# Performance work log

Hardware: AMD Instinct MI355X
Metric: run time of the kernel (lower is better)

## Reference

```python
import jax, jax.numpy as jnp
import numpy as np
import math

B, S, E = 2, 2048, 2048
H, NOPE, ROPE, V, KVR, DOWN = 16, 64, 32, 64, 256, 2
QKD = NOPE + ROPE
SCALE = QKD ** -0.5
LOW = 4


def setup_inputs() -> dict:
    key = jax.random.key(0)
    ks = jax.random.split(key, 8)
    def w(k, shape):
        return jax.random.normal(k, shape, jnp.float32) * 0.02
    return {
        "hidden_states": jax.random.normal(ks[0], (B, S, E), jnp.float32),
        "wq": w(ks[1], (H * QKD, E)),
        "wkv_a": w(ks[2], (KVR + ROPE, E)),
        "kv_ln_g": jnp.ones((KVR,), jnp.float32),
        "kv_ln_b": jnp.zeros((KVR,), jnp.float32),
        "wkv_b": w(ks[3], (H * (NOPE + V), KVR)),
        "wo": w(ks[4], (E, H * V)),
        "fc_c_w": w(ks[5], (KVR // LOW, KVR)),
        "fc_c_b": jnp.zeros((KVR // LOW,), jnp.float32),
        "fc_p_w": w(ks[6], (KVR // LOW, KVR)),
        "fc_p_b": jnp.zeros((KVR // LOW,), jnp.float32),
    }


def _layernorm(x, g, b, eps=1e-5):
    m = jnp.mean(x, -1, keepdims=True)
    v = jnp.var(x, -1, keepdims=True)
    return (x - m) * jax.lax.rsqrt(v + eps) * g + b


def _pos_enc(T, d):
    # sinusoidal PE: even dims sin, odd dims cos (interleaved)
    pos = jnp.arange(T, dtype=jnp.float32)[:, None]
    div = jnp.exp(jnp.arange(0, d, 2, dtype=jnp.float32) * (-math.log(10000.0) / d))
    ang = pos * div[None, :]
    return jnp.stack([jnp.sin(ang), jnp.cos(ang)], -1).reshape(T, d)


def _rope(x, cos, sin):
    # complex multiply on adjacent pairs, matching torch.view_as_complex path
    xr = x.reshape(x.shape[:-1] + (-1, 2))
    x0, x1 = xr[..., 0], xr[..., 1]
    return jnp.stack([x0 * cos - x1 * sin, x0 * sin + x1 * cos], -1).reshape(x.shape)


def reference(hidden_states, wq, wkv_a, kv_ln_g, kv_ln_b, wkv_b, wo,
              fc_c_w, fc_c_b, fc_p_w, fc_p_b):
    # q projection -> split nope / rope parts
    q = (hidden_states @ wq.T).reshape(B, S, H, QKD)
    q_nope, q_pe = q[..., :NOPE], q[..., NOPE:]
    # low-rank kv projection -> latent + shared rope key
    kv = hidden_states @ wkv_a.T
    kv_c, k_pe = kv[..., :KVR], kv[..., KVR:]
    kv_c = _layernorm(kv_c, kv_ln_g, kv_ln_b)
    # inline partial RoPE (position_ids = arange)
    pos = jnp.arange(S, dtype=jnp.float32)
    freqs = 1.0 / (10000.0 ** (jnp.arange(0, ROPE, 2, dtype=jnp.float32) / ROPE))
    ang = pos[:, None] * freqs[None, :]  # (S, ROPE//2)
    cos, sin = jnp.cos(ang), jnp.sin(ang)
    q_pe = _rope(q_pe, cos[None, :, None, :], sin[None, :, None, :])
    k_pe = _rope(k_pe, cos[None, :, :], sin[None, :, :])
    # hypernetwork gate (train path): C from downsampled PE, repeat_interleave
    t = -(-S // DOWN)
    P = _pos_enc(S, KVR)
    C = jnp.repeat(_pos_enc(t, KVR), DOWN, axis=0)[:S]
    C2 = C @ fc_c_w.T + fc_c_b
    P2 = P @ fc_p_w.T + fc_p_b
    Wg = jax.nn.sigmoid(C2 @ P2.T)  # (S, S)
    r = jnp.arange(S)
    chunk = ((r[:, None] // DOWN) == (r[None, :] // DOWN)) & \
            ((r[:, None] % DOWN) >= (r[None, :] % DOWN))
    Wg = Wg * chunk.astype(Wg.dtype)
    # temporally merged latent KV (simulated compressed cache)
    kv_t = jnp.einsum('ts,bsc->btc', Wg, kv_c)
    k_pe_t = jnp.einsum('ts,bsr->btr', Wg, k_pe)
    # absorbed wkv_b: q_nope into latent space
    wkv_b3 = wkv_b.reshape(H, NOPE + V, KVR)
    q_abs = jnp.einsum('bshd,hdc->bshc', q_nope, wkv_b3[:, :NOPE])
    scores = (jnp.einsum('bshc,btc->bsht', q_abs, kv_t)
              + jnp.einsum('bshr,btr->bsht', q_pe, k_pe_t)) * SCALE
    # stride-aware causal mask: chunk-boundary keys + diagonal
    visible = ((r[None, :] <= r[:, None]) & (((r[None, :] + 1) % DOWN) == 0)) | \
              (r[None, :] == r[:, None])
    mask = jnp.where(visible, 0.0, -1e9).astype(scores.dtype)
    attn = jax.nn.softmax(scores + mask[:, None, :], axis=-1)
    x = jnp.einsum('bsht,btc->bshc', attn, kv_t)
    out = jnp.einsum('bshc,hdc->bshd', x, wkv_b3[:, NOPE:]).reshape(B, S, H * V)
    return out @ wo.T
```

## Files before the change

kernel.cpp:

```cpp
#include <hip/hip_runtime.h>
#include <hip/hip_bf16.h>
#include <math.h>
#include <stdint.h>

#define B_ 2
#define S_ 2048
#define E_ 2048
#define H_ 16
#define NOPE_ 64
#define ROPE_ 32
#define V_ 64
#define KVR_ 256
#define QKD_ 96
#define SCALE_ 0.10206207261596577f

typedef __hip_bfloat16 bf16;
typedef __attribute__((ext_vector_type(8))) short short8;
typedef __attribute__((ext_vector_type(4))) short short4v;
typedef __attribute__((ext_vector_type(4))) float floatx4;

__device__ __forceinline__ float bf2f(bf16 v) { return __bfloat162float(v); }
__device__ __forceinline__ float s2f(short v) {
    bf16 h = *reinterpret_cast<bf16*>(&v);
    return __bfloat162float(h);
}
__device__ __forceinline__ short f2bf_s(float f) {
    bf16 h = __float2bfloat16(f);
    return *reinterpret_cast<short*>(&h);
}
__device__ __forceinline__ void store_c(float* C, size_t i, float v) { C[i] = v; }
__device__ __forceinline__ void store_c(bf16* C, size_t i, float v) { C[i] = __float2bfloat16(v); }

__device__ __forceinline__ void g2l16(const bf16* g, bf16* l) {
    __builtin_amdgcn_global_load_lds(
        (const __attribute__((address_space(1))) void*)g,
        (__attribute__((address_space(3))) void*)l,
        16, 0, 0);
}

#if __has_builtin(__builtin_amdgcn_mfma_f32_16x16x16_bf16)
#define HAVE_M16 1
#define MFMA16(a, b, c) __builtin_amdgcn_mfma_f32_16x16x16_bf16(a, b, c, 0, 0, 0)
#elif __has_builtin(__builtin_amdgcn_mfma_f32_16x16x16bf16_1k)
#define HAVE_M16 1
#define MFMA16(a, b, c) __builtin_amdgcn_mfma_f32_16x16x16bf16_1k(a, b, c, 0, 0, 0)
#else
#define HAVE_M16 0
#endif

__global__ __launch_bounds__(256) void conv_bf16_kernel(const float* __restrict__ src,
                                                        bf16* __restrict__ dst, int n8) {
    int i = blockIdx.x * 256 + threadIdx.x;
    if (i >= n8) return;
    float4 a = ((const float4*)src)[2 * i];
    float4 b = ((const float4*)src)[2 * i + 1];
    short8 r;
    r[0] = f2bf_s(a.x); r[1] = f2bf_s(a.y); r[2] = f2bf_s(a.z); r[3] = f2bf_s(a.w);
    r[4] = f2bf_s(b.x); r[5] = f2bf_s(b.y); r[6] = f2bf_s(b.z); r[7] = f2bf_s(b.w);
    ((short8*)dst)[i] = r;
}

__global__ __launch_bounds__(256) void conv_pad_wkva_kernel(const float* __restrict__ src,
                                                            bf16* __restrict__ dst) {
    int i = blockIdx.x * 256 + threadIdx.x;
    if (i >= 384 * 2048 / 8) return;
    int row = i >> 8;
    short8 r;
    if (row < 288) {
        float4 a = ((const float4*)src)[2 * i];
        float4 b = ((const float4*)src)[2 * i + 1];
        r[0] = f2bf_s(a.x); r[1] = f2bf_s(a.y); r[2] = f2bf_s(a.z); r[3] = f2bf_s(a.w);
        r[4] = f2bf_s(b.x); r[5] = f2bf_s(b.y); r[6] = f2bf_s(b.z); r[7] = f2bf_s(b.w);
    } else {
        for (int j = 0; j < 8; ++j) r[j] = 0;
    }
    ((short8*)dst)[i] = r;
}

__global__ __launch_bounds__(256) void transpose_wkvbT_kernel(const float* __restrict__ wkv_b,
                                                              bf16* __restrict__ wkvbT) {
    int h = blockIdx.x, c = threadIdx.x;
#pragma unroll
    for (int d0 = 0; d0 < 64; d0 += 8) {
        short8 v;
#pragma unroll
        for (int j = 0; j < 8; ++j) v[j] = f2bf_s(wkv_b[(size_t)(h * 128 + d0 + j) * 256 + c]);
        *(short8*)(void*)&wkvbT[((size_t)h * 256 + c) * 64 + d0] = v;
    }
}

template <typename TC>
__global__ __launch_bounds__(256, 2) void gemm_bt_lds(const bf16* __restrict__ A,
                                                      const bf16* __restrict__ Bm,
                                                      TC* __restrict__ C,
                                                      int M, int N, int K) {
    __shared__ bf16 Asf[128 * 32];
    __shared__ bf16 Bsf[128 * 32];
    int tid = threadIdx.x;
    int lane = tid & 63, w = tid >> 6;
    int q4 = lane >> 4, c16 = lane & 15;
    int wr = w >> 1, wc = w & 1;
    int m0 = blockIdx.y * 128, n0 = blockIdx.x * 128;
    floatx4 acc[4][4];
#pragma unroll
    for (int mi = 0; mi < 4; ++mi)
#pragma unroll
        for (int ni = 0; ni < 4; ++ni) acc[mi][ni] = (floatx4){0.f, 0.f, 0.f, 0.f};

    for (int k0 = 0; k0 < K; k0 += 32) {
        __syncthreads();
#pragma unroll
        for (int i = 0; i < 2; ++i) {
            int c = (w << 6) + lane + i * 256;
            int row = c >> 2, kc = c & 3;
            g2l16(&A[(size_t)(m0 + row) * K + k0 + kc * 8], &Asf[c * 8]);
            g2l16(&Bm[(size_t)(n0 + row) * K + k0 + kc * 8], &Bsf[c * 8]);
        }
        __syncthreads();
        short8 af[4], bfr[4];
#pragma unroll
        for (int mi = 0; mi < 4; ++mi)
            af[mi] = *(const short8*)(const void*)&Asf[(wr * 64 + mi * 16 + c16) * 32 + q4 * 8];
#pragma unroll
        for (int ni = 0; ni < 4; ++ni)
            bfr[ni] = *(const short8*)(const void*)&Bsf[(wc * 64 + ni * 16 + c16) * 32 + q4 * 8];
#pragma unroll
        for (int mi = 0; mi < 4; ++mi)
#pragma unroll
            for (int ni = 0; ni < 4; ++ni)
                acc[mi][ni] = __builtin_amdgcn_mfma_f32_16x16x32_bf16(af[mi], bfr[ni], acc[mi][ni], 0, 0, 0);
    }
#pragma unroll
    for (int mi = 0; mi < 4; ++mi)
#pragma unroll
        for (int ni = 0; ni < 4; ++ni)
#pragma unroll
            for (int r = 0; r < 4; ++r) {
                int row = m0 + wr * 64 + mi * 16 + q4 * 4 + r;
                int col = n0 + wc * 64 + ni * 16 + c16;
                store_c(C, (size_t)row * N + col, acc[mi][ni][r]);
            }
}

__global__ __launch_bounds__(256, 2) void gemm_qkv_fused(const bf16* __restrict__ A,
                                                         const bf16* __restrict__ Bq,
                                                         const bf16* __restrict__ Bkv,
                                                         bf16* __restrict__ Cq,
                                                         float* __restrict__ Ckv,
                                                         int K) {
    __shared__ bf16 Asf[128 * 32];
    __shared__ bf16 Bsf[128 * 32];
    int tid = threadIdx.x;
    int lane = tid & 63, w = tid >> 6;
    int q4 = lane >> 4, c16 = lane & 15;
    int wr = w >> 1, wc = w & 1;
    int bx = blockIdx.x;
    bool isq = bx < 12;
    const bf16* Bm = isq ? Bq : Bkv;
    int n0 = isq ? bx * 128 : (bx - 12) * 128;
    int m0 = blockIdx.y * 128;
    floatx4 acc[4][4];
#pragma unroll
    for (int mi = 0; mi < 4; ++mi)
#pragma unroll
        for (int ni = 0; ni < 4; ++ni) acc[mi][ni] = (floatx4){0.f, 0.f, 0.f, 0.f};

    for (int k0 = 0; k0 < K; k0 += 32) {
        __syncthreads();
#pragma unroll
        for (int i = 0; i < 2; ++i) {
            int c = (w << 6) + lane + i * 256;
            int row = c >> 2, kc = c & 3;
            g2l16(&A[(size_t)(m0 + row) * K + k0 + kc * 8], &Asf[c * 8]);
            g2l16(&Bm[(size_t)(n0 + row) * K + k0 + kc * 8], &Bsf[c * 8]);
        }
        __syncthreads();
        short8 af[4], bfr[4];
#pragma unroll
        for (int mi = 0; mi < 4; ++mi)
            af[mi] = *(const short8*)(const void*)&Asf[(wr * 64 + mi * 16 + c16) * 32 + q4 * 8];
#pragma unroll
        for (int ni = 0; ni < 4; ++ni)
            bfr[ni] = *(const short8*)(const void*)&Bsf[(wc * 64 + ni * 16 + c16) * 32 + q4 * 8];
#pragma unroll
        for (int mi = 0; mi < 4; ++mi)
#pragma unroll
            for (int ni = 0; ni < 4; ++ni)
                acc[mi][ni] = __builtin_amdgcn_mfma_f32_16x16x32_bf16(af[mi], bfr[ni], acc[mi][ni], 0, 0, 0);
    }
#pragma unroll
    for (int mi = 0; mi < 4; ++mi)
#pragma unroll
        for (int ni = 0; ni < 4; ++ni)
#pragma unroll
            for (int r = 0; r < 4; ++r) {
                int row = m0 + wr * 64 + mi * 16 + q4 * 4 + r;
                int col = n0 + wc * 64 + ni * 16 + c16;
                if (isq)
                    Cq[(size_t)row * 1536 + col] = __float2bfloat16(acc[mi][ni][r]);
                else
                    Ckv[(size_t)row * 384 + col] = acc[mi][ni][r];
            }
}

template <typename TC>
__global__ __launch_bounds__(256, 4) void gemm64_lds(const bf16* __restrict__ A, int lda, int aoffz,
                                                     const bf16* __restrict__ Bm, int ldb, int boffz,
                                                     TC* __restrict__ C, int ldc, int coffz,
                                                     int K, float scale) {
    int z = blockIdx.z;
    A += (size_t)z * aoffz;
    Bm += (size_t)z * boffz;
    C += (size_t)z * coffz;
    __shared__ bf16 Asf[64 * 32];
    __shared__ bf16 Bsf[64 * 32];
    int tid = threadIdx.x;
    int lane = tid & 63, w = tid >> 6;
    int q4 = lane >> 4, c16 = lane & 15;
    int m0 = blockIdx.y * 64, n0 = blockIdx.x * 64;
    floatx4 acc[4];
#pragma unroll
    for (int ni = 0; ni < 4; ++ni) acc[ni] = (floatx4){0.f, 0.f, 0.f, 0.f};
    int row = tid >> 2, kc = tid & 3;
    for (int k0 = 0; k0 < K; k0 += 32) {
        __syncthreads();
        g2l16(&A[(size_t)(m0 + row) * lda + k0 + kc * 8], &Asf[tid * 8]);
        g2l16(&Bm[(size_t)(n0 + row) * ldb + k0 + kc * 8], &Bsf[tid * 8]);
        __syncthreads();
        short8 af = *(const short8*)(const void*)&Asf[(w * 16 + c16) * 32 + q4 * 8];
#pragma unroll
        for (int ni = 0; ni < 4; ++ni) {
            short8 bfr = *(const short8*)(const void*)&Bsf[(ni * 16 + c16) * 32 + q4 * 8];
            acc[ni] = __builtin_amdgcn_mfma_f32_16x16x32_bf16(af, bfr, acc[ni], 0, 0, 0);
        }
    }
#pragma unroll
    for (int ni = 0; ni < 4; ++ni)
#pragma unroll
        for (int rr = 0; rr < 4; ++rr)
            store_c(C, (size_t)(m0 + w * 16 + q4 * 4 + rr) * ldc + n0 + ni * 16 + c16,
                    acc[ni][rr] * scale);
}

__global__ __launch_bounds__(256) void ln_rope_kernel(const float* __restrict__ kvraw,
                                                      const float* __restrict__ g,
                                                      const float* __restrict__ bta,
                                                      float* __restrict__ kv_c,
                                                      float* __restrict__ kpe) {
    int r = blockIdx.x;
    int tid = threadIdx.x;
    int lane = tid & 63, w = tid >> 6;
    float x = kvraw[(size_t)r * 384 + tid];
    float v1 = x, v2 = x * x;
#pragma unroll
    for (int o = 32; o; o >>= 1) { v1 += __shfl_down(v1, o); v2 += __shfl_down(v2, o); }
    __shared__ float s1[4], s2[4], stats[2];
    if (lane == 0) { s1[w] = v1; s2[w] = v2; }
    __syncthreads();
    if (tid == 0) {
        float S1 = s1[0] + s1[1] + s1[2] + s1[3];
        float S2 = s2[0] + s2[1] + s2[2] + s2[3];
        float mean = S1 / 256.0f;
        float var = S2 / 256.0f - mean * mean;
        stats[0] = mean;
        stats[1] = rsqrtf(var + 1e-5f);
    }
    __syncthreads();
    float y = (x - stats[0]) * stats[1] * g[tid] + bta[tid];
    kv_c[(size_t)r * 256 + tid] = y;
    if (tid < 16) {
        int j = tid;
        int s = r & (S_ - 1);
        float freq = expf(-(float)(2 * j) * 0.28782313662425572f);
        float ang = (float)s * freq;
        float c = cosf(ang), sn = sinf(ang);
        float x0 = kvraw[(size_t)r * 384 + 256 + 2 * j];
        float x1 = kvraw[(size_t)r * 384 + 256 + 2 * j + 1];
        kpe[(size_t)r * 32 + 2 * j]     = x0 * c - x1 * sn;
        kpe[(size_t)r * 32 + 2 * j + 1] = x0 * sn + x1 * c;
    }
}

__global__ __launch_bounds__(64) void c2p2_kernel(const float* __restrict__ fcw_c,
                                                  const float* __restrict__ fcb_c,
                                                  const float* __restrict__ fcw_p,
                                                  const float* __restrict__ fcb_p,
                                                  float* __restrict__ C2,
                                                  float* __restrict__ P2) {
    int t = blockIdx.x;
    int k = threadIdx.x;
    __shared__ float Crow[256], Prow[256];
    for (int i = k; i < 128; i += 64) {
        float div = expf(-(float)i * 0.07195578415606393f);
        float ap = (float)t * div;
        Prow[2 * i]     = sinf(ap);
        Prow[2 * i + 1] = cosf(ap);
        float ac = (float)(t >> 1) * div;
        Crow[2 * i]     = sinf(ac);
        Crow[2 * i + 1] = cosf(ac);
    }
    __syncthreads();
    float sc = fcb_c[k], sp = fcb_p[k];
    for (int c = 0; c < 256; ++c) {
        sc += Crow[c] * fcw_c[(size_t)k * 256 + c];
        sp += Prow[c] * fcw_p[(size_t)k * 256 + c];
    }
    C2[(size_t)t * 64 + k] = sc;
    P2[(size_t)t * 64 + k] = sp;
}

__global__ __launch_bounds__(256) void gates_kernel(const float* __restrict__ C2,
                                                    const float* __restrict__ P2,
                                                    float* __restrict__ g0,
                                                    float* __restrict__ g1) {
    int t = blockIdx.x * 256 + threadIdx.x;
    if (t >= S_) return;
    float d0 = 0.f;
    for (int k = 0; k < 64; ++k) d0 += C2[(size_t)t * 64 + k] * P2[(size_t)t * 64 + k];
    g0[t] = 1.0f / (1.0f + expf(-d0));
    float gg = 0.f;
    if (t & 1) {
        float d1 = 0.f;
        for (int k = 0; k < 64; ++k) d1 += C2[(size_t)t * 64 + k] * P2[(size_t)(t - 1) * 64 + k];
        gg = 1.0f / (1.0f + expf(-d1));
    }
    g1[t] = gg;
}

__global__ __launch_bounds__(256) void kve_kernel(const float* __restrict__ kv_c,
                                                  const float* __restrict__ kpe,
                                                  const float* __restrict__ g0,
                                                  const float* __restrict__ g1,
                                                  bf16* __restrict__ kve_full,
                                                  bf16* __restrict__ kvo) {
    int r = blockIdx.x, tid = threadIdx.x;
    int b = r >> 11, t = r & (S_ - 1);
    float a = g0[t], bb = g1[t];
    float v = a * kv_c[(size_t)r * 256 + tid];
    if (t & 1) v += bb * kv_c[(size_t)(r - 1) * 256 + tid];
    bf16 vb = __float2bfloat16(v);
    kve_full[(size_t)r * 288 + tid] = vb;
    if (t & 1) kvo[((size_t)b * 1024 + (t >> 1)) * 296 + tid] = vb;
    if (tid < 32) {
        float u = a * kpe[(size_t)r * 32 + tid];
        if (t & 1) u += bb * kpe[(size_t)(r - 1) * 32 + tid];
        bf16 ub = __float2bfloat16(u);
        kve_full[(size_t)r * 288 + 256 + tid] = ub;
        if (t & 1) kvo[((size_t)b * 1024 + (t >> 1)) * 296 + 256 + tid] = ub;
    }
}

__global__ __launch_bounds__(256) void kvoT2_kernel(const bf16* __restrict__ kvo,
                                                    bf16* __restrict__ kvoT) {
    int uch = blockIdx.x, b = blockIdx.y;
    int c = threadIdx.x;
    const bf16* src = kvo + ((size_t)b * 1024 + uch * 16) * 296 + c;
    short8 o0, o1;
#pragma unroll
    for (int j = 0; j < 8; ++j) o0[j] = *(const short*)&src[(size_t)j * 296];
#pragma unroll
    for (int j = 0; j < 8; ++j) o1[j] = *(const short*)&src[(size_t)(8 + j) * 296];
    bf16* dst = kvoT + (((size_t)b * 64 + uch) * 256 + c) * 16;
    *(short8*)(void*)dst = o0;
    *(short8*)(void*)(dst + 8) = o1;
}

__global__ __launch_bounds__(256) void rope_qe_kernel(const bf16* __restrict__ q,
                                                      bf16* __restrict__ qe) {
    int idx = blockIdx.x * 256 + threadIdx.x;
    if (idx >= B_ * S_ * H_ * 16) return;
    int j = idx & 15;
    int s = (idx >> 8) & (S_ - 1);
    float freq = expf(-(float)(2 * j) * 0.28782313662425572f);
    float ang = (float)s * freq;
    float c = cosf(ang), sn = sinf(ang);
    size_t row = idx >> 4;
    float a0 = bf2f(q[row * QKD_ + NOPE_ + 2 * j]);
    float a1 = bf2f(q[row * QKD_ + NOPE_ + 2 * j + 1]);
    qe[row * 288 + 256 + 2 * j]     = __float2bfloat16((a0 * c - a1 * sn) * SCALE_);
    qe[row * 288 + 256 + 2 * j + 1] = __float2bfloat16((a0 * sn + a1 * c) * SCALE_);
}

__global__ __launch_bounds__(256) void sscore_kernel(const bf16* __restrict__ qe,
                                                     const bf16* __restrict__ kve_full,
                                                     float* __restrict__ sscore) {
    int s = blockIdx.x, b = blockIdx.y;
    int tid = threadIdx.x;
    int h = tid >> 4, p = tid & 15;
    const bf16* qrow = qe + ((size_t)(b * S_ + s) * H_ + h) * 288;
    const bf16* krow = kve_full + (size_t)(b * S_ + s) * 288;
    float d = 0.f;
#pragma unroll
    for (int e = 0; e < 18; ++e) d += bf2f(qrow[p * 18 + e]) * bf2f(krow[p * 18 + e]);
    d += __shfl_xor(d, 1);
    d += __shfl_xor(d, 2);
    d += __shfl_xor(d, 4);
    d += __shfl_xor(d, 8);
    if (p == 0) sscore[((size_t)(b * S_ + s)) * H_ + h] = d;
}

__global__ __launch_bounds__(256, 3) void attn3_kernel(const bf16* __restrict__ qe,
                                                       const bf16* __restrict__ kvo,
                                                       const bf16* __restrict__ kvoT,
                                                       const bf16* __restrict__ kve_full,
                                                       const float* __restrict__ sscore,
                                                       bf16* __restrict__ xout) {
    int s0 = (int)(gridDim.x - 1 - blockIdx.x) * 4;
    int b = blockIdx.y;
    int tid = threadIdx.x;
    int lane = tid & 63, w = tid >> 6;
    int q4 = lane >> 4, c16 = lane & 15;
    int s = s0 + w;
    int Nodd = (s + 1) >> 1;
    int NoddMax = (s0 + 4) >> 1;
    int niterB = (NoddMax + 15) >> 4;

    __shared__ bf16 kvos[2][16][296];
    __shared__ bf16 kvoTs[2][256][24];
    __shared__ bf16 selfr[4][256];

    const bf16* kvob = kvo + (size_t)b * 1024 * 296;
    const bf16* kvoTb = kvoT + (size_t)b * 64 * 4096;

    if (tid < 128) {
        int rr = tid >> 5, ch = tid & 31;
        *(short8*)(void*)&selfr[rr][ch * 8] =
            *(const short8*)(const void*)&kve_full[(size_t)(b * S_ + s0 + rr) * 288 + ch * 8];
    }

    short8 qf[9];
    const bf16* qrow = qe + ((size_t)(b * S_ + s) * H_ + c16) * 288;
#pragma unroll
    for (int kk = 0; kk < 9; ++kk) qf[kk] = *(const short8*)(const void*)&qrow[kk * 32 + q4 * 8];

    floatx4 acc[16];
#pragma unroll
    for (int n = 0; n < 16; ++n) acc[n] = (floatx4){0.f, 0.f, 0.f, 0.f};
    float m_i = -1e30f, l_i = 0.f;

    short8 ra[3], rb[2];
    auto load_regs = [&](int t) {
        const short8* sa = (const short8*)(const void*)(kvob + (size_t)t * 16 * 296);
#pragma unroll
        for (int i = 0; i < 3; ++i) {
            int idx = tid + i * 256;
            if (idx < 592) ra[i] = sa[idx];
        }
        const short8* sb = (const short8*)(const void*)(kvoTb + (size_t)t * 4096);
#pragma unroll
        for (int i = 0; i < 2; ++i) rb[i] = sb[tid + i * 256];
    };
    auto write_lds = [&](int p) {
        short8* da = (short8*)(void*)&kvos[p][0][0];
#pragma unroll
        for (int i = 0; i < 3; ++i) {
            int idx = tid + i * 256;
            if (idx < 592) da[idx] = ra[i];
        }
#pragma unroll
        for (int i = 0; i < 2; ++i) {
            int idx = tid + i * 256;
            *(short8*)(void*)&kvoTs[p][idx >> 1][(idx & 1) * 8] = rb[i];
        }
    };

    load_regs(0);
    write_lds(0);
    if (niterB > 1) load_regs(1);
    __syncthreads();

    for (int it = 0; it < niterB; ++it) {
        int p = it & 1;
        if (it + 1 < niterB) {
            write_lds(1 - p);
            if (it + 2 < niterB) load_regs(it + 2);
        }
        int u0 = it * 16;
        floatx4 cf = (floatx4){0.f, 0.f, 0.f, 0.f};
#pragma unroll
        for (int kk = 0; kk < 9; ++kk) {
            short8 av = *(const short8*)(const void*)&kvos[p][c16][kk * 32 + q4 * 8];
            cf = __builtin_amdgcn_mfma_f32_16x16x32_bf16(av, qf[kk], cf, 0, 0, 0);
        }
        int ub = u0 + q4 * 4;
#pragma unroll
        for (int r = 0; r < 4; ++r)
            if (ub + r >= Nodd) cf[r] = -1e30f;
        float tmax = fmaxf(fmaxf(cf[0], cf[1]), fmaxf(cf[2], cf[3]));
        tmax = fmaxf(tmax, __shfl_xor(tmax, 16));
        tmax = fmaxf(tmax, __shfl_xor(tmax, 32));
        float mn = fmaxf(m_i, tmax);
        bool chg = mn > m_i;
        float al = __expf(m_i - mn);
        float p0 = __expf(cf[0] - mn), p1 = __expf(cf[1] - mn);
        float p2 = __expf(cf[2] - mn), p3 = __expf(cf[3] - mn);
        float rs = p0 + p1 + p2 + p3;
        rs += __shfl_xor(rs, 16);
        rs += __shfl_xor(rs, 32);
        l_i = l_i * al + rs;
        m_i = mn;
        if (__any(chg)) {
#pragma unroll
            for (int n = 0; n < 16; ++n) {
                acc[n][0] *= al; acc[n][1] *= al; acc[n][2] *= al; acc[n][3] *= al;
            }
        }
#if HAVE_M16
        short4v pfv;
        pfv[0] = f2bf_s(p0); pfv[1] = f2bf_s(p1); pfv[2] = f2bf_s(p2); pfv[3] = f2bf_s(p3);
#pragma unroll
        for (int n = 0; n < 16; ++n) {
            short4v a4 = *(const short4v*)(const void*)&kvoTs[p][n * 16 + c16][q4 * 4];
            acc[n] = MFMA16(a4, pfv, acc[n]);
        }
#else
        short8 pf;
        pf[0] = f2bf_s(p0); pf[1] = f2bf_s(p1); pf[2] = f2bf_s(p2); pf[3] = f2bf_s(p3);
        pf[4] = 0; pf[5] = 0; pf[6] = 0; pf[7] = 0;
#pragma unroll
        for (int n = 0; n < 16; ++n) {
            short4v a4 = *(const short4v*)(const void*)&kvoTs[p][n * 16 + c16][q4 * 4];
            short8 af;
            af[0] = a4[0]; af[1] = a4[1]; af[2] = a4[2]; af[3] = a4[3];
            af[4] = 0; af[5] = 0; af[6] = 0; af[7] = 0;
            acc[n] = __builtin_amdgcn_mfma_f32_16x16x32_bf16(af, pf, acc[n], 0, 0, 0);
        }
#endif
        __syncthreads();
    }

    if ((s & 1) == 0) {
        float scs = sscore[((size_t)(b * S_ + s)) * H_ + c16];
        float mn = fmaxf(m_i, scs);
        float al = __expf(m_i - mn);
        float pp = __expf(scs - mn);
        l_i = l_i * al + pp;
        m_i = mn;
#pragma unroll
        for (int n = 0; n < 16; ++n) {
            short4v kv4 = *(const short4v*)(const void*)&selfr[w][n * 16 + q4 * 4];
#pragma unroll
            for (int r = 0; r < 4; ++r)
                acc[n][r] = acc[n][r] * al + pp * s2f(kv4[r]);
        }
    }

    float invl = 1.0f / l_i;
    bf16* orow = xout + ((size_t)(b * S_ + s) * H_ + c16) * 256;
#pragma unroll
    for (int n = 0; n < 16; ++n) {
        short4v o;
        o[0] = f2bf_s(acc[n][0] * invl);
        o[1] = f2bf_s(acc[n][1] * invl);
        o[2] = f2bf_s(acc[n][2] * invl);
        o[3] = f2bf_s(acc[n][3] * invl);
        *(short4v*)(void*)&orow[n * 16 + q4 * 4] = o;
    }
}

extern "C" void kernel_launch(void* const* d_in, const int* in_sizes, int n_in,
                              void* d_out, int out_size, void* d_ws, size_t ws_size,
                              hipStream_t stream) {
    const float* hs     = (const float*)d_in[0];
    const float* wq     = (const float*)d_in[1];
    const float* wkv_a  = (const float*)d_in[2];
    const float* ln_g   = (const float*)d_in[3];
    const float* ln_b   = (const float*)d_in[4];
    const float* wkv_b  = (const float*)d_in[5];
    const float* wo     = (const float*)d_in[6];
    const float* fc_c_w = (const float*)d_in[7];
    const float* fc_c_b = (const float*)d_in[8];
    const float* fc_p_w = (const float*)d_in[9];
    const float* fc_p_b = (const float*)d_in[10];
    float* out = (float*)d_out;
    (void)in_sizes; (void)n_in; (void)out_size; (void)ws_size;

    const int M = B_ * S_;
    char* wsb = (char*)d_ws;
    size_t o = 0;
    auto alloc = [&](size_t bytes) { char* p = wsb + o; o += (bytes + 255) & ~(size_t)255; return p; };

    bf16* qe = (bf16*)alloc((size_t)M * H_ * 288 * 2);
    char* region2 = alloc((size_t)M * H_ * 256 * 2);
    bf16* hs_bf    = (bf16*)region2;
    bf16* wq_bf    = (bf16*)(region2 + (size_t)M * E_ * 2);
    bf16* wkva_pad = (bf16*)(region2 + (size_t)M * E_ * 2 + (size_t)1536 * E_ * 2);
    bf16* x_bf     = (bf16*)region2;
    char* region3 = alloc((size_t)M * 1536 * 2);
    bf16* q_bf    = (bf16*)region3;
    bf16* outp_bf = (bf16*)region3;
    float* kvraw = (float*)alloc((size_t)M * 384 * 4);
    float* kv_c  = (float*)alloc((size_t)M * 256 * 4);
    float* kpe   = (float*)alloc((size_t)M * 32 * 4);
    bf16* wo_bf   = (bf16*)alloc((size_t)E_ * 1024 * 2);
    bf16* wkvb_bf = (bf16*)alloc((size_t)2048 * 256 * 2);
    bf16* wkvbT   = (bf16*)alloc((size_t)H_ * 256 * 64 * 2);
    bf16* kve_full = (bf16*)alloc((size_t)M * 288 * 2);
    bf16* kvo      = (bf16*)alloc((size_t)B_ * 1024 * 296 * 2);
    bf16* kvoT     = (bf16*)alloc((size_t)B_ * 64 * 4096 * 2);
    float* sscore  = (float*)alloc((size_t)M * H_ * 4);
    float* C2 = (float*)alloc((size_t)S_ * 64 * 4);
    float* P2 = (float*)alloc((size_t)S_ * 64 * 4);
    float* g0 = (float*)alloc(S_ * 4);
    float* g1 = (float*)alloc(S_ * 4);

    conv_bf16_kernel<<<(M * E_ / 8 + 255) / 256, 256, 0, stream>>>(hs, hs_bf, M * E_ / 8);
    conv_bf16_kernel<<<(1536 * E_ / 8 + 255) / 256, 256, 0, stream>>>(wq, wq_bf, 1536 * E_ / 8);
    conv_bf16_kernel<<<(E_ * 1024 / 8 + 255) / 256, 256, 0, stream>>>(wo, wo_bf, E_ * 1024 / 8);
    conv_bf16_kernel<<<(2048 * 256 / 8 + 255) / 256, 256, 0, stream>>>(wkv_b, wkvb_bf, 2048 * 256 / 8);
    conv_pad_wkva_kernel<<<(384 * 2048 / 8 + 255) / 256, 256, 0, stream>>>(wkv_a, wkva_pad);
    transpose_wkvbT_kernel<<<H_, 256, 0, stream>>>(wkv_b, wkvbT);
    gemm_qkv_fused<<<dim3(15, M / 128), 256, 0, stream>>>(hs_bf, wq_bf, wkva_pad, q_bf, kvraw, E_);
    ln_rope_kernel<<<M, 256, 0, stream>>>(kvraw, ln_g, ln_b, kv_c, kpe);
    c2p2_kernel<<<S_, 64, 0, stream>>>(fc_c_w, fc_c_b, fc_p_w, fc_p_b, C2, P2);
    gates_kernel<<<(S_ + 255) / 256, 256, 0, stream>>>(C2, P2, g0, g1);
    kve_kernel<<<M, 256, 0, stream>>>(kv_c, kpe, g0, g1, kve_full, kvo);
    kvoT2_kernel<<<dim3(64, B_), 256, 0, stream>>>(kvo, kvoT);
    gemm64_lds<bf16><<<dim3(256 / 64, M / 64, H_), 256, 0, stream>>>(
        q_bf, H_ * QKD_, QKD_, wkvbT, 64, 256 * 64, qe, H_ * 288, 288, 64, SCALE_);
    rope_qe_kernel<<<(M * H_ * 16 + 255) / 256, 256, 0, stream>>>(q_bf, qe);
    sscore_kernel<<<dim3(S_, B_), 256, 0, stream>>>(qe, kve_full, sscore);
    attn3_kernel<<<dim3(S_ / 4, B_), 256, 0, stream>>>(qe, kvo, kvoT, kve_full, sscore, x_bf);
    gemm64_lds<bf16><<<dim3(1, M / 64, H_), 256, 0, stream>>>(
        x_bf, H_ * 256, 256, wkvb_bf + (size_t)64 * 256, 256, 128 * 256, outp_bf, 1024, 64, 256, 1.0f);
    gemm_bt_lds<float><<<dim3(E_ / 128, M / 128), 256, 0, stream>>>(outp_bf, wo_bf, out, M, E_, 1024);
}
```

Before: 395.2 us.

## Widen attention key tiles to 32 with direct global-to-LDS staging

```diff
diff --git a/kernel.cpp b/kernel.cpp
--- a/kernel.cpp
+++ b/kernel.cpp
@@ -37,16 +37,6 @@
         (__attribute__((address_space(3))) void*)l,
         16, 0, 0);
 }
-
-#if __has_builtin(__builtin_amdgcn_mfma_f32_16x16x16_bf16)
-#define HAVE_M16 1
-#define MFMA16(a, b, c) __builtin_amdgcn_mfma_f32_16x16x16_bf16(a, b, c, 0, 0, 0)
-#elif __has_builtin(__builtin_amdgcn_mfma_f32_16x16x16bf16_1k)
-#define HAVE_M16 1
-#define MFMA16(a, b, c) __builtin_amdgcn_mfma_f32_16x16x16bf16_1k(a, b, c, 0, 0, 0)
-#else
-#define HAVE_M16 0
-#endif
 
 __global__ __launch_bounds__(256) void conv_bf16_kernel(const float* __restrict__ src,
                                                         bf16* __restrict__ dst, int n8) {
@@ -350,19 +340,23 @@
     }
 }
 
-__global__ __launch_bounds__(256) void kvoT2_kernel(const bf16* __restrict__ kvo,
-                                                    bf16* __restrict__ kvoT) {
+__global__ __launch_bounds__(256) void kvoT32_kernel(const bf16* __restrict__ kvo,
+                                                     bf16* __restrict__ kvoT) {
     int uch = blockIdx.x, b = blockIdx.y;
     int c = threadIdx.x;
-    const bf16* src = kvo + ((size_t)b * 1024 + uch * 16) * 296 + c;
-    short8 o0, o1;
-#pragma unroll
-    for (int j = 0; j < 8; ++j) o0[j] = *(const short*)&src[(size_t)j * 296];
-#pragma unroll
-    for (int j = 0; j < 8; ++j) o1[j] = *(const short*)&src[(size_t)(8 + j) * 296];
-    bf16* dst = kvoT + (((size_t)b * 64 + uch) * 256 + c) * 16;
-    *(short8*)(void*)dst = o0;
-    *(short8*)(void*)(dst + 8) = o1;
+    const bf16* src = kvo + ((size_t)b * 1024 + uch * 32) * 296 + c;
+    short v[32];
+#pragma unroll
+    for (int j = 0; j < 32; ++j) v[j] = *(const short*)&src[(size_t)j * 296];
+    bf16* dst = kvoT + (((size_t)b * 32 + uch) * 256 + c) * 32;
+#pragma unroll
+    for (int q = 0; q < 4; ++q) {
+        short8 o;
+#pragma unroll
+        for (int jj = 0; jj < 8; ++jj)
+            o[jj] = (jj < 4) ? v[4 * q + jj] : v[16 + 4 * q + (jj - 4)];
+        *(short8*)(void*)&dst[q * 8] = o;
+    }
 }
 
 __global__ __launch_bounds__(256) void rope_qe_kernel(const bf16* __restrict__ q,
@@ -399,7 +393,7 @@
     if (p == 0) sscore[((size_t)(b * S_ + s)) * H_ + h] = d;
 }
 
-__global__ __launch_bounds__(256, 3) void attn3_kernel(const bf16* __restrict__ qe,
+__global__ __launch_bounds__(256, 3) void attn4_kernel(const bf16* __restrict__ qe,
                                                        const bf16* __restrict__ kvo,
                                                        const bf16* __restrict__ kvoT,
                                                        const bf16* __restrict__ kve_full,
@@ -413,14 +407,14 @@
     int s = s0 + w;
     int Nodd = (s + 1) >> 1;
     int NoddMax = (s0 + 4) >> 1;
-    int niterB = (NoddMax + 15) >> 4;
-
-    __shared__ bf16 kvos[2][16][296];
-    __shared__ bf16 kvoTs[2][256][24];
+    int niter = (NoddMax + 31) >> 5;
+
+    __shared__ bf16 kvos[32][296];
+    __shared__ bf16 kvts[256][32];
     __shared__ bf16 selfr[4][256];
 
     const bf16* kvob = kvo + (size_t)b * 1024 * 296;
-    const bf16* kvoTb = kvoT + (size_t)b * 64 * 4096;
+    const bf16* kvoTb = kvoT + (size_t)b * 32 * 8192;
 
     if (tid < 128) {
         int rr = tid >> 5, ch = tid & 31;
@@ -438,63 +432,60 @@
     for (int n = 0; n < 16; ++n) acc[n] = (floatx4){0.f, 0.f, 0.f, 0.f};
     float m_i = -1e30f, l_i = 0.f;
 
-    short8 ra[3], rb[2];
-    auto load_regs = [&](int t) {
-        const short8* sa = (const short8*)(const void*)(kvob + (size_t)t * 16 * 296);
-#pragma unroll
-        for (int i = 0; i < 3; ++i) {
-            int idx = tid + i * 256;
-            if (idx < 592) ra[i] = sa[idx];
-        }
-        const short8* sb = (const short8*)(const void*)(kvoTb + (size_t)t * 4096);
-#pragma unroll
-        for (int i = 0; i < 2; ++i) rb[i] = sb[tid + i * 256];
+    auto stage = [&](int t) {
+        const bf16* sa = kvob + (size_t)t * 32 * 296;
+        bf16* la = &kvos[0][0];
+#pragma unroll
+        for (int i = 0; i < 4; ++i)
+            g2l16(&sa[(size_t)(tid + i * 256) * 8], &la[(size_t)(tid + i * 256) * 8]);
+        if (tid < 160) g2l16(&sa[(size_t)(tid + 1024) * 8], &la[(size_t)(tid + 1024) * 8]);
+        const bf16* sb = kvoTb + (size_t)t * 8192;
+        bf16* lb = &kvts[0][0];
+#pragma unroll
+        for (int i = 0; i < 4; ++i)
+            g2l16(&sb[(size_t)(tid + i * 256) * 8], &lb[(size_t)(tid + i * 256) * 8]);
     };
-    auto write_lds = [&](int p) {
-        short8* da = (short8*)(void*)&kvos[p][0][0];
-#pragma unroll
-        for (int i = 0; i < 3; ++i) {
-            int idx = tid + i * 256;
-            if (idx < 592) da[idx] = ra[i];
-        }
-#pragma unroll
-        for (int i = 0; i < 2; ++i) {
-            int idx = tid + i * 256;
-            *(short8*)(void*)&kvoTs[p][idx >> 1][(idx & 1) * 8] = rb[i];
-        }
-    };
-
-    load_regs(0);
-    write_lds(0);
-    if (niterB > 1) load_regs(1);
+
+    stage(0);
     __syncthreads();
 
-    for (int it = 0; it < niterB; ++it) {
-        int p = it & 1;
-        if (it + 1 < niterB) {
-            write_lds(1 - p);
-            if (it + 2 < niterB) load_regs(it + 2);
-        }
-        int u0 = it * 16;
-        floatx4 cf = (floatx4){0.f, 0.f, 0.f, 0.f};
+    for (int it = 0; it < niter; ++it) {
+        int u0 = it * 32;
+        floatx4 ca0 = (floatx4){0.f, 0.f, 0.f, 0.f}, ca1 = (floatx4){0.f, 0.f, 0.f, 0.f};
+        floatx4 cb0 = (floatx4){0.f, 0.f, 0.f, 0.f}, cb1 = (floatx4){0.f, 0.f, 0.f, 0.f};
 #pragma unroll
         for (int kk = 0; kk < 9; ++kk) {
-            short8 av = *(const short8*)(const void*)&kvos[p][c16][kk * 32 + q4 * 8];
-            cf = __builtin_amdgcn_mfma_f32_16x16x32_bf16(av, qf[kk], cf, 0, 0, 0);
-        }
-        int ub = u0 + q4 * 4;
-#pragma unroll
-        for (int r = 0; r < 4; ++r)
-            if (ub + r >= Nodd) cf[r] = -1e30f;
-        float tmax = fmaxf(fmaxf(cf[0], cf[1]), fmaxf(cf[2], cf[3]));
+            short8 avA = *(const short8*)(const void*)&kvos[c16][kk * 32 + q4 * 8];
+            short8 avB = *(const short8*)(const void*)&kvos[16 + c16][kk * 32 + q4 * 8];
+            if (kk & 1) {
+                ca1 = __builtin_amdgcn_mfma_f32_16x16x32_bf16(avA, qf[kk], ca1, 0, 0, 0);
+                cb1 = __builtin_amdgcn_mfma_f32_16x16x32_bf16(avB, qf[kk], cb1, 0, 0, 0);
+            } else {
+                ca0 = __builtin_amdgcn_mfma_f32_16x16x32_bf16(avA, qf[kk], ca0, 0, 0, 0);
+                cb0 = __builtin_amdgcn_mfma_f32_16x16x32_bf16(avB, qf[kk], cb0, 0, 0, 0);
+            }
+        }
+        floatx4 cA = ca0 + ca1;
+        floatx4 cB = cb0 + cb1;
+        int kA = u0 + q4 * 4;
+        int kB = u0 + 16 + q4 * 4;
+#pragma unroll
+        for (int r = 0; r < 4; ++r) {
+            if (kA + r >= Nodd) cA[r] = -1e30f;
+            if (kB + r >= Nodd) cB[r] = -1e30f;
+        }
+        float tmax = fmaxf(fmaxf(fmaxf(cA[0], cA[1]), fmaxf(cA[2], cA[3])),
+                           fmaxf(fmaxf(cB[0], cB[1]), fmaxf(cB[2], cB[3])));
         tmax = fmaxf(tmax, __shfl_xor(tmax, 16));
         tmax = fmaxf(tmax, __shfl_xor(tmax, 32));
         float mn = fmaxf(m_i, tmax);
         bool chg = mn > m_i;
         float al = __expf(m_i - mn);
-        float p0 = __expf(cf[0] - mn), p1 = __expf(cf[1] - mn);
-        float p2 = __expf(cf[2] - mn), p3 = __expf(cf[3] - mn);
-        float rs = p0 + p1 + p2 + p3;
+        float pA0 = __expf(cA[0] - mn), pA1 = __expf(cA[1] - mn);
+        float pA2 = __expf(cA[2] - mn), pA3 = __expf(cA[3] - mn);
+        float pB0 = __expf(cB[0] - mn), pB1 = __expf(cB[1] - mn);
+        float pB2 = __expf(cB[2] - mn), pB3 = __expf(cB[3] - mn);
+        float rs = (pA0 + pA1 + pA2 + pA3) + (pB0 + pB1 + pB2 + pB3);
         rs += __shfl_xor(rs, 16);
         rs += __shfl_xor(rs, 32);
         l_i = l_i * al + rs;
@@ -505,27 +496,16 @@
                 acc[n][0] *= al; acc[n][1] *= al; acc[n][2] *= al; acc[n][3] *= al;
             }
         }
-#if HAVE_M16
-        short4v pfv;
-        pfv[0] = f2bf_s(p0); pfv[1] = f2bf_s(p1); pfv[2] = f2bf_s(p2); pfv[3] = f2bf_s(p3);
+        short8 pf;
+        pf[0] = f2bf_s(pA0); pf[1] = f2bf_s(pA1); pf[2] = f2bf_s(pA2); pf[3] = f2bf_s(pA3);
+        pf[4] = f2bf_s(pB0); pf[5] = f2bf_s(pB1); pf[6] = f2bf_s(pB2); pf[7] = f2bf_s(pB3);
 #pragma unroll
         for (int n = 0; n < 16; ++n) {
-            short4v a4 = *(const short4v*)(const void*)&kvoTs[p][n * 16 + c16][q4 * 4];
-            acc[n] = MFMA16(a4, pfv, acc[n]);
-        }
-#else
-        short8 pf;
-        pf[0] = f2bf_s(p0); pf[1] = f2bf_s(p1); pf[2] = f2bf_s(p2); pf[3] = f2bf_s(p3);
-        pf[4] = 0; pf[5] = 0; pf[6] = 0; pf[7] = 0;
-#pragma unroll
-        for (int n = 0; n < 16; ++n) {
-            short4v a4 = *(const short4v*)(const void*)&kvoTs[p][n * 16 + c16][q4 * 4];
-            short8 af;
-            af[0] = a4[0]; af[1] = a4[1]; af[2] = a4[2]; af[3] = a4[3];
-            af[4] = 0; af[5] = 0; af[6] = 0; af[7] = 0;
-            acc[n] = __builtin_amdgcn_mfma_f32_16x16x32_bf16(af, pf, acc[n], 0, 0, 0);
-        }
-#endif
+            short8 a8 = *(const short8*)(const void*)&kvts[n * 16 + c16][q4 * 8];
+            acc[n] = __builtin_amdgcn_mfma_f32_16x16x32_bf16(a8, pf, acc[n], 0, 0, 0);
+        }
+        __syncthreads();
+        if (it + 1 < niter) stage(it + 1);
         __syncthreads();
     }
 
@@ -597,7 +577,7 @@
     bf16* wkvbT   = (bf16*)alloc((size_t)H_ * 256 * 64 * 2);
     bf16* kve_full = (bf16*)alloc((size_t)M * 288 * 2);
     bf16* kvo      = (bf16*)alloc((size_t)B_ * 1024 * 296 * 2);
-    bf16* kvoT     = (bf16*)alloc((size_t)B_ * 64 * 4096 * 2);
+    bf16* kvoT     = (bf16*)alloc((size_t)B_ * 32 * 8192 * 2);
     float* sscore  = (float*)alloc((size_t)M * H_ * 4);
     float* C2 = (float*)alloc((size_t)S_ * 64 * 4);
     float* P2 = (float*)alloc((size_t)S_ * 64 * 4);
@@ -615,12 +595,12 @@
     c2p2_kernel<<<S_, 64, 0, stream>>>(fc_c_w, fc_c_b, fc_p_w, fc_p_b, C2, P2);
     gates_kernel<<<(S_ + 255) / 256, 256, 0, stream>>>(C2, P2, g0, g1);
     kve_kernel<<<M, 256, 0, stream>>>(kv_c, kpe, g0, g1, kve_full, kvo);
-    kvoT2_kernel<<<dim3(64, B_), 256, 0, stream>>>(kvo, kvoT);
+    kvoT32_kernel<<<dim3(32, B_), 256, 0, stream>>>(kvo, kvoT);
     gemm64_lds<bf16><<<dim3(256 / 64, M / 64, H_), 256, 0, stream>>>(
         q_bf, H_ * QKD_, QKD_, wkvbT, 64, 256 * 64, qe, H_ * 288, 288, 64, SCALE_);
     rope_qe_kernel<<<(M * H_ * 16 + 255) / 256, 256, 0, stream>>>(q_bf, qe);
     sscore_kernel<<<dim3(S_, B_), 256, 0, stream>>>(qe, kve_full, sscore);
-    attn3_kernel<<<dim3(S_ / 4, B_), 256, 0, stream>>>(qe, kvo, kvoT, kve_full, sscore, x_bf);
+    attn4_kernel<<<dim3(S_ / 4, B_), 256, 0, stream>>>(qe, kvo, kvoT, kve_full, sscore, x_bf);
     gemm64_lds<bf16><<<dim3(1, M / 64, H_), 256, 0, stream>>>(
         x_bf, H_ * 256, 256, wkvb_bf + (size_t)64 * 256, 256, 128 * 256, outp_bf, 1024, 64, 256, 1.0f);
     gemm_bt_lds<float><<<dim3(E_ / 128, M / 128), 256, 0, stream>>>(outp_bf, wo_bf, out, M, E_, 1024);
```

New measurement: 363.5 us. -8.0%, faster.
